# Kernel tuning notes

Measured on AMD Instinct MI355X. Metric: run time of the kernel, lower is better.

## Reference

```python
import jax, jax.numpy as jnp
import numpy as np

DECAY = 0.99
EPS = 1e-05
N_EMBED = 4096  # codebook_size
DIM = 128       # latent_size
N = 131072      # flattened batch of vectors


def setup_inputs() -> dict:
    key = jax.random.key(0)
    k1, k2, k3, k4 = jax.random.split(key, 4)
    x = jax.random.normal(k1, (N, DIM), dtype=jnp.float32)
    embed = jax.random.normal(k2, (DIM, N_EMBED), dtype=jnp.float32)
    cluster_size = jax.random.uniform(k3, (N_EMBED,), dtype=jnp.float32)
    embed_avg = jax.random.normal(k4, (DIM, N_EMBED), dtype=jnp.float32)
    return {"x": x, "embed": embed, "cluster_size": cluster_size, "embed_avg": embed_avg}


def reference(x, embed, cluster_size, embed_avg):
    dist = (x * x).sum(1, keepdims=True) - 2.0 * (x @ embed) + (embed * embed).sum(0, keepdims=True)
    embed_ind = jnp.argmin(dist, axis=1)  # == (-dist).max(1) index

    # Quantize with the PRE-update codebook (matches torch ordering)
    quantize = jnp.take(embed.T, embed_ind, axis=0)  # [N, DIM]

    # EMA statistics via scatter-reduce (one-hot sum / x^T @ one-hot)
    ones = jnp.ones_like(embed_ind, dtype=x.dtype)
    embed_onehot_sum = jax.ops.segment_sum(ones, embed_ind, num_segments=N_EMBED)        # [K]
    embed_sum = jax.ops.segment_sum(x, embed_ind, num_segments=N_EMBED).T               # [DIM, K]

    cluster_size_new = cluster_size * DECAY + (1.0 - DECAY) * embed_onehot_sum
    embed_avg_new = embed_avg * DECAY + (1.0 - DECAY) * embed_sum

    # low_usage_threshold == -1 -> reinit branch disabled; just count small clusters
    n_small_clusters = (cluster_size_new < 1.0).sum()

    # Laplace-smoothed normalization of the EMA codebook
    n = cluster_size_new.sum()
    cs_norm = (cluster_size_new + EPS) / (n + N_EMBED * EPS) * n
    embed_new = embed_avg_new / cs_norm[None, :]

    quant_loss = jnp.mean((jax.lax.stop_gradient(quantize) - x) ** 2)
    quantize_st = x + jax.lax.stop_gradient(quantize - x)  # straight-through

    return quantize_st, quant_loss, n_small_clusters, embed_ind, embed_new, cluster_size_new, embed_avg_new
```

## Files before the change

kernel.cpp:

```cpp
#include <hip/hip_runtime.h>

constexpr int   NVEC  = 131072;
constexpr int   DIMC  = 128;
constexpr int   KC    = 4096;
constexpr float DECAYC = 0.99f;
constexpr float OMDECAY = 0.01f;
constexpr float EPSC  = 1e-5f;
constexpr float MARGIN1 = 0.4f;
constexpr float MARGIN2 = 0.02f;

typedef __bf16 v8bf __attribute__((ext_vector_type(8)));
typedef float  v4f  __attribute__((ext_vector_type(4)));

__device__ __forceinline__ void async_copy16(const void* gp, void* lds_wave_base, int lane) {
#if __has_builtin(__builtin_amdgcn_global_load_lds)
    __builtin_amdgcn_global_load_lds(
        (const __attribute__((address_space(1))) unsigned int*)gp,
        (__attribute__((address_space(3))) unsigned int*)lds_wave_base, 16, 0, 0);
#else
    ((v8bf*)lds_wave_base)[lane] = *(const v8bf*)gp;
#endif
}

__global__ __launch_bounds__(256) void split_e_kernel(const float* __restrict__ embed,
                                                      __bf16* __restrict__ ehT,
                                                      __bf16* __restrict__ elT,
                                                      float* __restrict__ nhe2) {
    __shared__ __bf16 sh_h[64 * 130];
    __shared__ __bf16 sh_l[64 * 130];
    __shared__ float  sh_n[4][64];
    const int tid = threadIdx.x;
    const int kbase = blockIdx.x * 64;
    const int kloc = tid & 63;
    float nacc = 0.f;
    for (int it = 0; it < 32; ++it) {
        int d = it * 4 + (tid >> 6);
        float v = embed[(size_t)d * KC + kbase + kloc];
        __bf16 h = (__bf16)v;
        __bf16 l = (__bf16)(v - (float)h);
        sh_h[kloc * 130 + d] = h;
        sh_l[kloc * 130 + d] = l;
        nacc = fmaf(v, v, nacc);
    }
    sh_n[tid >> 6][kloc] = nacc;
    __syncthreads();
    if (tid < 64)
        nhe2[kbase + tid] = -0.5f * (sh_n[0][tid] + sh_n[1][tid] + sh_n[2][tid] + sh_n[3][tid]);
    for (int it = 0; it < 32; ++it) {
        int idx = it * 256 + tid;
        int k = idx >> 7;
        int d = idx & 127;
        ehT[(size_t)(kbase + k) * DIMC + d] = sh_h[k * 130 + d];
        elT[(size_t)(kbase + k) * DIMC + d] = sh_l[k * 130 + d];
    }
}

__global__ __launch_bounds__(256, 2) void phase1_kernel(
    const float* __restrict__ x, const __bf16* __restrict__ ehT,
    const float* __restrict__ nhe2,
    float* __restrict__ out_indf, int* __restrict__ ws_ind, float* __restrict__ ws_gap)
{
    __shared__ v8bf E[1024];
    const int tid  = threadIdx.x;
    const int wave = tid >> 6;
    const int lane = tid & 63;
    const int c    = lane & 15;
    const int q    = lane >> 4;
    const int rowBase = blockIdx.x * 128 + wave * 32;

    v8bf ah[2][4];
#pragma unroll
    for (int t = 0; t < 2; ++t)
#pragma unroll
        for (int s = 0; s < 4; ++s) {
            const float* p = x + (size_t)(rowBase + t * 16 + c) * DIMC + s * 32 + q * 8;
            float4 v0 = *reinterpret_cast<const float4*>(p);
            float4 v1 = *reinterpret_cast<const float4*>(p + 4);
            float vv[8] = {v0.x, v0.y, v0.z, v0.w, v1.x, v1.y, v1.z, v1.w};
            v8bf h;
#pragma unroll
            for (int j = 0; j < 8; ++j) h[j] = (__bf16)vv[j];
            ah[t][s] = h;
        }

    const __bf16* ph = ehT + (size_t)(tid & 15) * DIMC + (tid >> 4) * 8;

    float b1[8], b2[8]; int i1[8];
#pragma unroll
    for (int s = 0; s < 8; ++s) { b1[s] = -3.4e38f; b2[s] = -3.4e38f; i1[s] = 0; }

    for (int chunk = 0; chunk < KC / 64; ++chunk) {
        float nhc[4];
#pragma unroll
        for (int t4 = 0; t4 < 4; ++t4) nhc[t4] = nhe2[chunk * 64 + t4 * 16 + c];
#pragma unroll
        for (int it = 0; it < 4; ++it)
            async_copy16(ph + (size_t)it * 16 * DIMC, &E[it * 256 + wave * 64], lane);
        ph += (size_t)64 * DIMC;
        __syncthreads();

#pragma unroll
        for (int ct = 0; ct < 4; ++ct) {
            const float nh = nhc[ct];
            v4f acc0 = {nh, nh, nh, nh};
            v4f acc1 = {nh, nh, nh, nh};
#pragma unroll
            for (int s = 0; s < 4; ++s) {
                v8bf bh = E[ct * 256 + s * 64 + lane];
                acc0 = __builtin_amdgcn_mfma_f32_16x16x32_bf16(ah[0][s], bh, acc0, 0, 0, 0);
                acc1 = __builtin_amdgcn_mfma_f32_16x16x32_bf16(ah[1][s], bh, acc1, 0, 0, 0);
            }
            const int colG = chunk * 64 + ct * 16 + c;
#pragma unroll
            for (int r = 0; r < 4; ++r) {
                float sc = acc0[r];
                float ob = b1[r];
                b2[r] = __builtin_amdgcn_fmed3f(ob, b2[r], sc);
                b1[r] = fmaxf(ob, sc);
                i1[r] = (sc > ob) ? colG : i1[r];
                float sc1 = acc1[r];
                float ob1 = b1[4 + r];
                b2[4 + r] = __builtin_amdgcn_fmed3f(ob1, b2[4 + r], sc1);
                b1[4 + r] = fmaxf(ob1, sc1);
                i1[4 + r] = (sc1 > ob1) ? colG : i1[4 + r];
            }
        }
        __syncthreads();
    }

#pragma unroll
    for (int off = 1; off < 16; off <<= 1) {
#pragma unroll
        for (int s = 0; s < 8; ++s) {
            float ob1 = __shfl_xor(b1[s], off, 64);
            int   oi1 = __shfl_xor(i1[s], off, 64);
            float ob2 = __shfl_xor(b2[s], off, 64);
            if (ob1 > b1[s] || (ob1 == b1[s] && oi1 < i1[s])) {
                b2[s] = fmaxf(b1[s], ob2); b1[s] = ob1; i1[s] = oi1;
            } else {
                b2[s] = fmaxf(b2[s], ob1);
            }
        }
    }
    if (c == 0) {
#pragma unroll
        for (int s = 0; s < 8; ++s) {
            int t = s >> 2, r = s & 3;
            int row = rowBase + t * 16 + q * 4 + r;
            ws_ind[row]   = i1[s];
            out_indf[row] = (float)i1[s];
            ws_gap[row]   = b1[s] - b2[s];
        }
    }
}

__global__ __launch_bounds__(256) void fh_kernel(const float* __restrict__ ws_gap,
                                                 const int* __restrict__ ws_ind,
                                                 int* __restrict__ ws_nflag,
                                                 int* __restrict__ ws_list,
                                                 int* __restrict__ cnt) {
    int n = blockIdx.x * 256 + threadIdx.x;
    if (ws_gap[n] < MARGIN1) {
        int p = atomicAdd(ws_nflag, 1);
        ws_list[p] = n;
    } else {
        atomicAdd(&cnt[ws_ind[n]], 1);
    }
}

__global__ __launch_bounds__(256, 2) void rescore_mfma_kernel(
    const float* __restrict__ x, const __bf16* __restrict__ ehT,
    const __bf16* __restrict__ elT, const float* __restrict__ nhe2,
    const int* __restrict__ ws_list, const int* __restrict__ ws_nflag,
    float* __restrict__ out_indf, int* __restrict__ ws_ind,
    int* __restrict__ ws_nflag2, int* __restrict__ ws_list2, int* __restrict__ cnt)
{
    const int nflag = *ws_nflag;
    if (blockIdx.x * 128 >= nflag) return;

    __shared__ v8bf E[2048];
    const int tid  = threadIdx.x;
    const int wave = tid >> 6;
    const int lane = tid & 63;
    const int c    = lane & 15;
    const int q    = lane >> 4;
    const int gBase = blockIdx.x * 128 + wave * 32;

    v8bf ah[2][4], al[2][4];
#pragma unroll
    for (int t = 0; t < 2; ++t) {
        int gi  = gBase + t * 16 + c;
        int row = ws_list[gi < nflag ? gi : nflag - 1];
#pragma unroll
        for (int s = 0; s < 4; ++s) {
            const float* p = x + (size_t)row * DIMC + s * 32 + q * 8;
            float4 v0 = *reinterpret_cast<const float4*>(p);
            float4 v1 = *reinterpret_cast<const float4*>(p + 4);
            float vv[8] = {v0.x, v0.y, v0.z, v0.w, v1.x, v1.y, v1.z, v1.w};
            v8bf h, l;
#pragma unroll
            for (int j = 0; j < 8; ++j) {
                __bf16 hh = (__bf16)vv[j];
                h[j] = hh;
                l[j] = (__bf16)(vv[j] - (float)hh);
            }
            ah[t][s] = h; al[t][s] = l;
        }
    }

    const __bf16* ph = ehT + (size_t)(tid & 15) * DIMC + (tid >> 4) * 8;
    const __bf16* pl = elT + (size_t)(tid & 15) * DIMC + (tid >> 4) * 8;

    float b1[8], b2[8]; int i1[8];
#pragma unroll
    for (int s = 0; s < 8; ++s) { b1[s] = -3.4e38f; b2[s] = -3.4e38f; i1[s] = 0; }

    for (int chunk = 0; chunk < KC / 64; ++chunk) {
        float nhc[4];
#pragma unroll
        for (int t4 = 0; t4 < 4; ++t4) nhc[t4] = nhe2[chunk * 64 + t4 * 16 + c];
#pragma unroll
        for (int it = 0; it < 4; ++it) {
            async_copy16(ph + (size_t)it * 16 * DIMC, &E[it * 256 + wave * 64], lane);
            async_copy16(pl + (size_t)it * 16 * DIMC, &E[1024 + it * 256 + wave * 64], lane);
        }
        ph += (size_t)64 * DIMC;
        pl += (size_t)64 * DIMC;
        __syncthreads();

#pragma unroll
        for (int ct = 0; ct < 4; ++ct) {
            const float nh = nhc[ct];
            v4f acc0 = {nh, nh, nh, nh};
            v4f acc1 = {nh, nh, nh, nh};
#pragma unroll
            for (int s = 0; s < 4; ++s) {
                v8bf bh = E[ct * 256 + s * 64 + lane];
                v8bf bl = E[1024 + ct * 256 + s * 64 + lane];
                acc0 = __builtin_amdgcn_mfma_f32_16x16x32_bf16(ah[0][s], bh, acc0, 0, 0, 0);
                acc1 = __builtin_amdgcn_mfma_f32_16x16x32_bf16(ah[1][s], bh, acc1, 0, 0, 0);
                acc0 = __builtin_amdgcn_mfma_f32_16x16x32_bf16(al[0][s], bh, acc0, 0, 0, 0);
                acc1 = __builtin_amdgcn_mfma_f32_16x16x32_bf16(al[1][s], bh, acc1, 0, 0, 0);
                acc0 = __builtin_amdgcn_mfma_f32_16x16x32_bf16(ah[0][s], bl, acc0, 0, 0, 0);
                acc1 = __builtin_amdgcn_mfma_f32_16x16x32_bf16(ah[1][s], bl, acc1, 0, 0, 0);
            }
            const int colG = chunk * 64 + ct * 16 + c;
#pragma unroll
            for (int r = 0; r < 4; ++r) {
                float sc = acc0[r];
                float ob = b1[r];
                b2[r] = __builtin_amdgcn_fmed3f(ob, b2[r], sc);
                b1[r] = fmaxf(ob, sc);
                i1[r] = (sc > ob) ? colG : i1[r];
                float sc1 = acc1[r];
                float ob1 = b1[4 + r];
                b2[4 + r] = __builtin_amdgcn_fmed3f(ob1, b2[4 + r], sc1);
                b1[4 + r] = fmaxf(ob1, sc1);
                i1[4 + r] = (sc1 > ob1) ? colG : i1[4 + r];
            }
        }
        __syncthreads();
    }

#pragma unroll
    for (int off = 1; off < 16; off <<= 1) {
#pragma unroll
        for (int s = 0; s < 8; ++s) {
            float ob1 = __shfl_xor(b1[s], off, 64);
            int   oi1 = __shfl_xor(i1[s], off, 64);
            float ob2 = __shfl_xor(b2[s], off, 64);
            if (ob1 > b1[s] || (ob1 == b1[s] && oi1 < i1[s])) {
                b2[s] = fmaxf(b1[s], ob2); b1[s] = ob1; i1[s] = oi1;
            } else {
                b2[s] = fmaxf(b2[s], ob1);
            }
        }
    }
    if (c == 0) {
#pragma unroll
        for (int s = 0; s < 8; ++s) {
            int t = s >> 2, r = s & 3;
            int gi = gBase + t * 16 + q * 4 + r;
            if (gi < nflag) {
                int row = ws_list[gi];
                ws_ind[row]   = i1[s];
                out_indf[row] = (float)i1[s];
                if (b1[s] - b2[s] < MARGIN2) {
                    int p = atomicAdd(ws_nflag2, 1);
                    ws_list2[p] = row;
                } else {
                    atomicAdd(&cnt[i1[s]], 1);
                }
            }
        }
    }
}

__global__ __launch_bounds__(256) void rescore_exact_kernel(
    const float* __restrict__ x, const float* __restrict__ embed,
    const float* __restrict__ nhe2, const int* __restrict__ ws_list,
    const int* __restrict__ ws_nflag, int* __restrict__ ws_ind,
    float* __restrict__ out_indf, int* __restrict__ cnt)
{
    __shared__ float xs[16][128];
    __shared__ float redv[4][16];
    __shared__ int   redi[4][16];
    const int tid  = threadIdx.x;
    const int lane = tid & 63;
    const int wave = tid >> 6;
    const int nflag = *ws_nflag;

    for (int g = blockIdx.x; g * 16 < nflag; g += gridDim.x) {
        const int base = g * 16;
        const int cntg = min(16, nflag - base);
        __syncthreads();
#pragma unroll
        for (int it = 0; it < 2; ++it) {
            int idx = it * 256 + tid;
            int r   = idx >> 5;
            int d4  = (idx & 31) * 4;
            int row = ws_list[base + (r < cntg ? r : 0)];
            float4 v = *reinterpret_cast<const float4*>(x + (size_t)row * DIMC + d4);
            *reinterpret_cast<float4*>(&xs[r][d4]) = v;
        }
        __syncthreads();

        float b1[16]; int i1[16];
#pragma unroll
        for (int r = 0; r < 16; ++r) { b1[r] = -3.4e38f; i1[r] = 0; }

#pragma unroll 1
        for (int iter = 0; iter < 4; ++iter) {
            const int col4 = iter * 1024 + tid * 4;
            float4 acc[16];
#pragma unroll
            for (int r = 0; r < 16; ++r) acc[r] = make_float4(0.f, 0.f, 0.f, 0.f);
#pragma unroll 4
            for (int d = 0; d < DIMC; ++d) {
                float4 ev = *reinterpret_cast<const float4*>(embed + (size_t)d * KC + col4);
#pragma unroll
                for (int r = 0; r < 16; ++r) {
                    float xv = xs[r][d];
                    acc[r].x = fmaf(ev.x, xv, acc[r].x);
                    acc[r].y = fmaf(ev.y, xv, acc[r].y);
                    acc[r].z = fmaf(ev.z, xv, acc[r].z);
                    acc[r].w = fmaf(ev.w, xv, acc[r].w);
                }
            }
            float4 nh = *reinterpret_cast<const float4*>(nhe2 + col4);
#pragma unroll
            for (int r = 0; r < 16; ++r) {
                float s0 = acc[r].x + nh.x;
                float s1 = acc[r].y + nh.y;
                float s2 = acc[r].z + nh.z;
                float s3 = acc[r].w + nh.w;
                if (s0 > b1[r]) { b1[r] = s0; i1[r] = col4 + 0; }
                if (s1 > b1[r]) { b1[r] = s1; i1[r] = col4 + 1; }
                if (s2 > b1[r]) { b1[r] = s2; i1[r] = col4 + 2; }
                if (s3 > b1[r]) { b1[r] = s3; i1[r] = col4 + 3; }
            }
        }
#pragma unroll
        for (int off = 1; off < 64; off <<= 1)
#pragma unroll
            for (int r = 0; r < 16; ++r) {
                float ob = __shfl_xor(b1[r], off, 64);
                int   oi = __shfl_xor(i1[r], off, 64);
                if (ob > b1[r] || (ob == b1[r] && oi < i1[r])) { b1[r] = ob; i1[r] = oi; }
            }
        if (lane == 0)
#pragma unroll
            for (int r = 0; r < 16; ++r) { redv[wave][r] = b1[r]; redi[wave][r] = i1[r]; }
        __syncthreads();
        if (tid < cntg) {
            float bv = redv[0][tid]; int bi = redi[0][tid];
#pragma unroll
            for (int w = 1; w < 4; ++w) {
                float ov = redv[w][tid]; int oi = redi[w][tid];
                if (ov > bv || (ov == bv && oi < bi)) { bv = ov; bi = oi; }
            }
            int row = ws_list[base + tid];
            ws_ind[row]   = bi;
            out_indf[row] = (float)bi;
            atomicAdd(&cnt[bi], 1);
        }
    }
}

__global__ __launch_bounds__(1024) void scan_kernel(const int* __restrict__ cnt,
                                                    int* __restrict__ start,
                                                    int* __restrict__ cursor) {
    __shared__ int sh[1024];
    const int t = threadIdx.x;
    int4 c = *reinterpret_cast<const int4*>(cnt + t * 4);
    int s = c.x + c.y + c.z + c.w;
    sh[t] = s;
    __syncthreads();
    for (int off = 1; off < 1024; off <<= 1) {
        int v = (t >= off) ? sh[t - off] : 0;
        __syncthreads();
        sh[t] += v;
        __syncthreads();
    }
    int s0 = (t == 0) ? 0 : sh[t - 1];
    start[t * 4 + 0] = s0; cursor[t * 4 + 0] = s0; s0 += c.x;
    start[t * 4 + 1] = s0; cursor[t * 4 + 1] = s0; s0 += c.y;
    start[t * 4 + 2] = s0; cursor[t * 4 + 2] = s0; s0 += c.z;
    start[t * 4 + 3] = s0; cursor[t * 4 + 3] = s0;
}

__global__ __launch_bounds__(256) void bucket_kernel(const int* __restrict__ ind,
                                                     int* __restrict__ cursor,
                                                     int* __restrict__ sorted) {
    int n = blockIdx.x * 256 + threadIdx.x;
    int p = atomicAdd(&cursor[ind[n]], 1);
    sorted[p] = n;
}

__global__ __launch_bounds__(128) void cluster_sum_kernel(
    const float* __restrict__ x, const float* __restrict__ embed,
    const int* __restrict__ sorted, const int* __restrict__ start,
    const int* __restrict__ cnt, float* __restrict__ quant_out,
    float* __restrict__ ws_sum, float* __restrict__ ws_lpart)
{
    const int k = blockIdx.x;
    const int d = threadIdx.x;
    const int s0 = start[k];
    const int c  = cnt[k];
    const float e = embed[(size_t)d * KC + k];
    __shared__ int rows[256];

    float a0 = 0.f, a1 = 0.f, a2 = 0.f, a3 = 0.f;
    float l0 = 0.f, l1 = 0.f, l2 = 0.f, l3 = 0.f;

    for (int base = 0; base < c; base += 256) {
        int m = min(256, c - base);
        __syncthreads();
        if (d < m)        rows[d] = sorted[s0 + base + d];
        if (d + 128 < m)  rows[d + 128] = sorted[s0 + base + d + 128];
        __syncthreads();
        int i = 0;
        for (; i + 4 <= m; i += 4) {
            int r0 = rows[i + 0], r1 = rows[i + 1], r2 = rows[i + 2], r3 = rows[i + 3];
            float x0 = x[(size_t)r0 * DIMC + d];
            float x1 = x[(size_t)r1 * DIMC + d];
            float x2 = x[(size_t)r2 * DIMC + d];
            float x3 = x[(size_t)r3 * DIMC + d];
            float d0 = e - x0, d1 = e - x1, d2 = e - x2, d3 = e - x3;
            a0 += x0; a1 += x1; a2 += x2; a3 += x3;
            l0 = fmaf(d0, d0, l0); l1 = fmaf(d1, d1, l1);
            l2 = fmaf(d2, d2, l2); l3 = fmaf(d3, d3, l3);
            quant_out[(size_t)r0 * DIMC + d] = x0 + d0;
            quant_out[(size_t)r1 * DIMC + d] = x1 + d1;
            quant_out[(size_t)r2 * DIMC + d] = x2 + d2;
            quant_out[(size_t)r3 * DIMC + d] = x3 + d3;
        }
        for (; i < m; ++i) {
            int r0 = rows[i];
            float x0 = x[(size_t)r0 * DIMC + d];
            float d0 = e - x0;
            a0 += x0;
            l0 = fmaf(d0, d0, l0);
            quant_out[(size_t)r0 * DIMC + d] = x0 + d0;
        }
    }
    float acc  = (a0 + a1) + (a2 + a3);
    float loss = (l0 + l1) + (l2 + l3);
    ws_sum[(size_t)d * KC + k] = acc;

#pragma unroll
    for (int off = 32; off >= 1; off >>= 1) loss += __shfl_down(loss, off, 64);
    __shared__ float red[2];
    if ((d & 63) == 0) red[d >> 6] = loss;
    __syncthreads();
    if (d == 0) ws_lpart[k] = red[0] + red[1];
}

__global__ __launch_bounds__(1024) void finalize_kernel(
    const float* __restrict__ cs, const int* __restrict__ cnt,
    const float* __restrict__ ws_lpart,
    float* __restrict__ out_loss, float* __restrict__ out_nsmall,
    float* __restrict__ out_csn, float* __restrict__ ws_inv)
{
    const int tid = threadIdx.x;
    float csn_loc[4];
    float lsum = 0.f, lsmall = 0.f, lloss = 0.f;
#pragma unroll
    for (int i = 0; i < 4; ++i) {
        int k = tid + i * 1024;
        float csn = cs[k] * DECAYC + OMDECAY * (float)cnt[k];
        out_csn[k] = csn;
        csn_loc[i] = csn;
        lsum += csn;
        lsmall += (csn < 1.f) ? 1.f : 0.f;
        lloss += ws_lpart[k];
    }
#pragma unroll
    for (int off = 32; off >= 1; off >>= 1) {
        lsum   += __shfl_down(lsum, off, 64);
        lsmall += __shfl_down(lsmall, off, 64);
        lloss  += __shfl_down(lloss, off, 64);
    }
    __shared__ float sh1[16], sh2[16], sh3[16];
    __shared__ float ntot_s;
    if ((tid & 63) == 0) { sh1[tid >> 6] = lsum; sh2[tid >> 6] = lsmall; sh3[tid >> 6] = lloss; }
    __syncthreads();
    if (tid == 0) {
        float tot = 0.f, sm = 0.f, lo = 0.f;
        for (int w = 0; w < 16; ++w) { tot += sh1[w]; sm += sh2[w]; lo += sh3[w]; }
        ntot_s = tot;
        out_nsmall[0] = sm;
        out_loss[0] = lo * (1.0f / ((float)NVEC * (float)DIMC));
    }
    __syncthreads();
    float ntot = ntot_s;
    float scale = (ntot + (float)KC * EPSC) / ntot;
#pragma unroll
    for (int i = 0; i < 4; ++i) {
        int k = tid + i * 1024;
        ws_inv[k] = scale / (csn_loc[i] + EPSC);
    }
}

__global__ __launch_bounds__(256) void ema_embed_kernel(
    const float* __restrict__ ea, const float* __restrict__ ws_sum,
    const float* __restrict__ ws_inv, float* __restrict__ out_embed_new,
    float* __restrict__ out_ean)
{
    size_t i4 = ((size_t)blockIdx.x * 256 + threadIdx.x) * 4;
    float4 a = *reinterpret_cast<const float4*>(ea + i4);
    float4 s = *reinterpret_cast<const float4*>(ws_sum + i4);
    int k = (int)(i4 & (KC - 1));
    float4 inv = *reinterpret_cast<const float4*>(ws_inv + k);
    float e0 = a.x * DECAYC + OMDECAY * s.x;
    float e1 = a.y * DECAYC + OMDECAY * s.y;
    float e2 = a.z * DECAYC + OMDECAY * s.z;
    float e3 = a.w * DECAYC + OMDECAY * s.w;
    *reinterpret_cast<float2*>(out_ean + i4)     = make_float2(e0, e1);
    *reinterpret_cast<float2*>(out_ean + i4 + 2) = make_float2(e2, e3);
    *reinterpret_cast<float2*>(out_embed_new + i4)     = make_float2(e0 * inv.x, e1 * inv.y);
    *reinterpret_cast<float2*>(out_embed_new + i4 + 2) = make_float2(e2 * inv.z, e3 * inv.w);
}

extern "C" void kernel_launch(void* const* d_in, const int* in_sizes, int n_in,
                              void* d_out, int out_size, void* d_ws, size_t ws_size,
                              hipStream_t stream) {
    const float* x     = (const float*)d_in[0];
    const float* embed = (const float*)d_in[1];
    const float* cs    = (const float*)d_in[2];
    const float* ea    = (const float*)d_in[3];

    float* out  = (float*)d_out;
    float* out0 = out;
    float* out1 = out + 16777216;
    float* out2 = out + 16777217;
    float* out3 = out + 16777218;
    float* out4 = out + 16908290;
    float* out5 = out + 17432578;
    float* out6 = out + 17436674;

    float* ws       = (float*)d_ws;
    float* ws_sum   = ws;
    int*   ws_nflag = (int*)(ws + 528385);
    float* ws_inv   = ws + 528388;
    float* nhe2     = ws + 532484;
    int*   ws_cnt_i  = (int*)(ws + 540676);
    int*   ws_nflag2 = (int*)(ws + 544772);
    int*   ws_list2  = (int*)(ws + 548868);
    int*   ws_ind   = (int*)(ws + 1060868);
    float* ws_gap   = ws + 1191940;
    int*   ws_list  = (int*)(ws + 1323012);
    __bf16* ehT     = (__bf16*)(ws + 1454084);
    __bf16* elT     = (__bf16*)(ws + 1716228);
    int*   ws_sorted = (int*)(ws + 1454084);
    int*   ws_start  = (int*)(ws + 1720324);
    int*   ws_cursor = (int*)(ws + 1724420);
    float* ws_lpart  = ws + 1728516;

    hipMemsetAsync(ws_nflag, 0, sizeof(int), stream);
    hipMemsetAsync(ws_nflag2, 0, sizeof(int), stream);
    hipMemsetAsync(ws_cnt_i, 0, KC * sizeof(int), stream);

    hipLaunchKernelGGL(split_e_kernel,   dim3(KC / 64), dim3(256), 0, stream,
                       embed, ehT, elT, nhe2);
    hipLaunchKernelGGL(phase1_kernel,    dim3(NVEC / 128), dim3(256), 0, stream,
                       x, ehT, nhe2, out3, ws_ind, ws_gap);

    hipLaunchKernelGGL(fh_kernel,        dim3(NVEC / 256), dim3(256), 0, stream,
                       ws_gap, ws_ind, ws_nflag, ws_list, ws_cnt_i);
    hipLaunchKernelGGL(rescore_mfma_kernel, dim3(NVEC / 128), dim3(256), 0, stream,
                       x, ehT, elT, nhe2, ws_list, ws_nflag,
                       out3, ws_ind, ws_nflag2, ws_list2, ws_cnt_i);
    hipLaunchKernelGGL(rescore_exact_kernel, dim3(512), dim3(256), 0, stream,
                       x, embed, nhe2, ws_list2, ws_nflag2, ws_ind, out3, ws_cnt_i);

    hipLaunchKernelGGL(scan_kernel,   dim3(1), dim3(1024), 0, stream, ws_cnt_i, ws_start, ws_cursor);
    hipLaunchKernelGGL(bucket_kernel, dim3(NVEC / 256), dim3(256), 0, stream,
                       ws_ind, ws_cursor, ws_sorted);
    hipLaunchKernelGGL(cluster_sum_kernel, dim3(KC), dim3(128), 0, stream,
                       x, embed, ws_sorted, ws_start, ws_cnt_i, out0, ws_sum, ws_lpart);

    hipLaunchKernelGGL(finalize_kernel, dim3(1), dim3(1024), 0, stream,
                       cs, ws_cnt_i, ws_lpart, out1, out2, out5, ws_inv);
    hipLaunchKernelGGL(ema_embed_kernel, dim3((DIMC * KC) / 1024), dim3(256), 0, stream,
                       ea, ws_sum, ws_inv, out4, out6);
}
```

Baseline: 846.0 us.

## Split each cluster's rows across eight thread groups in cluster_sum_kernel

The cluster-sum kernel goes from 128 to 1024 threads per block. Eight groups of 128 threads each handle a 32-row slice of every 256-row chunk, and their per-dimension sums and loss are then combined through shared-memory reductions. The aim is more memory-level parallelism on the gather/scatter of x rows, and to keep large clusters from serialising on one 128-thread block. The costs are idle groups for small clusters (average about 32 rows), extra shared-memory reductions and syncs, and lower occupancy per CU from the large blocks.

New measurement: 686.4 us. 1.23x faster.

```diff
diff --git a/kernel.cpp b/kernel.cpp
--- a/kernel.cpp
+++ b/kernel.cpp
@@ -417,63 +417,76 @@
     sorted[p] = n;
 }
 
-__global__ __launch_bounds__(128) void cluster_sum_kernel(
+__global__ __launch_bounds__(1024) void cluster_sum_kernel(
     const float* __restrict__ x, const float* __restrict__ embed,
     const int* __restrict__ sorted, const int* __restrict__ start,
     const int* __restrict__ cnt, float* __restrict__ quant_out,
     float* __restrict__ ws_sum, float* __restrict__ ws_lpart)
 {
-    const int k = blockIdx.x;
-    const int d = threadIdx.x;
-    const int s0 = start[k];
-    const int c  = cnt[k];
+    const int k   = blockIdx.x;
+    const int tid = threadIdx.x;
+    const int d   = tid & 127;
+    const int grp = tid >> 7;
+    const int s0  = start[k];
+    const int c   = cnt[k];
     const float e = embed[(size_t)d * KC + k];
-    __shared__ int rows[256];
-
-    float a0 = 0.f, a1 = 0.f, a2 = 0.f, a3 = 0.f;
-    float l0 = 0.f, l1 = 0.f, l2 = 0.f, l3 = 0.f;
+    __shared__ int   rows[256];
+    __shared__ float partial[8][128];
+    __shared__ float lred[16];
+
+    float asum = 0.f;
+    float loss = 0.f;
 
     for (int base = 0; base < c; base += 256) {
         int m = min(256, c - base);
         __syncthreads();
-        if (d < m)        rows[d] = sorted[s0 + base + d];
-        if (d + 128 < m)  rows[d + 128] = sorted[s0 + base + d + 128];
-        __syncthreads();
-        int i = 0;
-        for (; i + 4 <= m; i += 4) {
+        if (tid < m) rows[tid] = sorted[s0 + base + tid];
+        __syncthreads();
+        int lo = grp * 32;
+        int hi = min(lo + 32, m);
+        int i = lo;
+        for (; i + 4 <= hi; i += 4) {
             int r0 = rows[i + 0], r1 = rows[i + 1], r2 = rows[i + 2], r3 = rows[i + 3];
             float x0 = x[(size_t)r0 * DIMC + d];
             float x1 = x[(size_t)r1 * DIMC + d];
             float x2 = x[(size_t)r2 * DIMC + d];
             float x3 = x[(size_t)r3 * DIMC + d];
             float d0 = e - x0, d1 = e - x1, d2 = e - x2, d3 = e - x3;
-            a0 += x0; a1 += x1; a2 += x2; a3 += x3;
-            l0 = fmaf(d0, d0, l0); l1 = fmaf(d1, d1, l1);
-            l2 = fmaf(d2, d2, l2); l3 = fmaf(d3, d3, l3);
+            asum += x0; asum += x1; asum += x2; asum += x3;
+            loss = fmaf(d0, d0, loss); loss = fmaf(d1, d1, loss);
+            loss = fmaf(d2, d2, loss); loss = fmaf(d3, d3, loss);
             quant_out[(size_t)r0 * DIMC + d] = x0 + d0;
             quant_out[(size_t)r1 * DIMC + d] = x1 + d1;
             quant_out[(size_t)r2 * DIMC + d] = x2 + d2;
             quant_out[(size_t)r3 * DIMC + d] = x3 + d3;
         }
-        for (; i < m; ++i) {
+        for (; i < hi; ++i) {
             int r0 = rows[i];
             float x0 = x[(size_t)r0 * DIMC + d];
             float d0 = e - x0;
-            a0 += x0;
-            l0 = fmaf(d0, d0, l0);
+            asum += x0;
+            loss = fmaf(d0, d0, loss);
             quant_out[(size_t)r0 * DIMC + d] = x0 + d0;
         }
     }
-    float acc  = (a0 + a1) + (a2 + a3);
-    float loss = (l0 + l1) + (l2 + l3);
-    ws_sum[(size_t)d * KC + k] = acc;
-
+
+    partial[grp][d] = asum;
 #pragma unroll
     for (int off = 32; off >= 1; off >>= 1) loss += __shfl_down(loss, off, 64);
-    __shared__ float red[2];
-    if ((d & 63) == 0) red[d >> 6] = loss;
+    if ((tid & 63) == 0) lred[tid >> 6] = loss;
     __syncthreads();
-    if (d == 0) ws_lpart[k] = red[0] + red[1];
+    if (tid < 128) {
+        float s = partial[0][tid];
+#pragma unroll
+        for (int g2 = 1; g2 < 8; ++g2) s += partial[g2][tid];
+        ws_sum[(size_t)tid * KC + k] = s;
+    }
+    if (tid == 0) {
+        float L = 0.f;
+#pragma unroll
+        for (int w = 0; w < 16; ++w) L += lred[w];
+        ws_lpart[k] = L;
+    }
 }
 
 __global__ __launch_bounds__(1024) void finalize_kernel(
@@ -597,7 +610,7 @@
     hipLaunchKernelGGL(scan_kernel,   dim3(1), dim3(1024), 0, stream, ws_cnt_i, ws_start, ws_cursor);
     hipLaunchKernelGGL(bucket_kernel, dim3(NVEC / 256), dim3(256), 0, stream,
                        ws_ind, ws_cursor, ws_sorted);
-    hipLaunchKernelGGL(cluster_sum_kernel, dim3(KC), dim3(128), 0, stream,
+    hipLaunchKernelGGL(cluster_sum_kernel, dim3(KC), dim3(1024), 0, stream,
                        x, embed, ws_sorted, ws_start, ws_cnt_i, out0, ws_sum, ws_lpart);
 
     hipLaunchKernelGGL(finalize_kernel, dim3(1), dim3(1024), 0, stream,
```
